# Kernel tuning notes

Hardware: AMD Instinct MI355X
Metric: run time of the kernel (lower is better)

Reference implementation:

```python
import jax, jax.numpy as jnp
import numpy as np

N_ATOMS = 4096
N_ANGLES = 200000


def setup_inputs() -> dict:
    key = jax.random.key(0)
    k1, k2, k3, k4, k5 = jax.random.split(key, 5)
    # pairwise unit direction vectors [N, N, 3]
    vec = jax.random.normal(k1, (N_ATOMS, N_ATOMS, 3), dtype=jnp.float32)
    vec = vec / jnp.linalg.norm(vec, axis=-1, keepdims=True)
    # pairwise distances [N, N], strictly positive
    dist = jax.random.uniform(k2, (N_ATOMS, N_ATOMS), dtype=jnp.float32) * 2.0 + 0.5
    # angle triplets [A, 3]
    coord_idx = jax.random.randint(k3, (N_ANGLES, 3), 0, N_ATOMS)
    # per-angle parameters: k0 (force const) and theta0 (equilibrium angle, rad)
    k0 = jax.random.uniform(k4, (N_ANGLES,), dtype=jnp.float32) * 100.0
    theta0 = jax.random.uniform(k5, (N_ANGLES,), dtype=jnp.float32) * np.float32(np.pi)
    params = jnp.stack([k0, theta0], axis=1)
    forces_out = jnp.zeros((N_ATOMS, 3), dtype=jnp.float32)
    return {
        "dist_mat": dist,
        "vector_mat": vec,
        "forces_out": forces_out,
        "params": params,
        "coord_idx": coord_idx,
        "calc_energy": 1,
        "calc_forces": 1,
    }


def reference(dist_mat, vector_mat, forces_out, params, coord_idx, calc_energy, calc_forces):
    k0 = params[:, 0]
    theta0 = params[:, 1]
    a1 = coord_idx[:, 0]
    a2 = coord_idx[:, 1]
    a3 = coord_idx[:, 2]

    vec21 = vector_mat[a2, a1]            # [A, 3]
    vec23 = vector_mat[a2, a3]            # [A, 3]
    dist21 = dist_mat[a2, a1]             # [A]
    dist23 = dist_mat[a2, a3]             # [A]

    cos_theta = jnp.clip(jnp.sum(vec21 * vec23, axis=1), -1.0, 1.0)
    theta = jnp.arccos(cos_theta)
    delta_theta = theta - theta0

    if calc_energy:
        energy = jnp.sum(k0 * delta_theta * delta_theta)
    else:
        energy = jnp.zeros([1], dtype=forces_out.dtype)

    forces = forces_out
    if calc_forces:
        sin_theta = jnp.sqrt(1.0 - cos_theta * cos_theta)
        # matches torch nan_to_num(nan=0.0): zero out coef where sin_theta == 0
        coef = jnp.where(sin_theta > 0.0,
                         -2.0 * k0 * delta_theta / jnp.maximum(sin_theta, 1e-12),
                         0.0)
        force0 = coef[:, None] * (cos_theta[:, None] * vec21 - vec23) / dist21[:, None]
        force2 = coef[:, None] * (cos_theta[:, None] * vec23 - vec21) / dist23[:, None]
        force1 = -(force0 + force2)
        forces = forces.at[a1].add(force0).at[a2].add(force1).at[a3].add(force2)

    return energy, forces
```

## Files before the change

kernel.cpp:

```cpp
#include <hip/hip_runtime.h>


#define NB 256
#define NT 1024

__global__ void init_out_kernel(float* __restrict__ out,
                                const float* __restrict__ forces0,
                                int nf) {
    int j = blockIdx.x * blockDim.x + threadIdx.x;
    if (j == 0) out[0] = 0.0f;
    if (j < nf) out[1 + j] = forces0[j];
}

template <bool USE_WS>
__global__ void __launch_bounds__(NT)
angle_fused_kernel(const float*  __restrict__ dist,
                   const float*  __restrict__ vec,
                   const float2* __restrict__ params,
                   const int*    __restrict__ cidx,
                   const int*    __restrict__ ce_p,
                   const int*    __restrict__ cf_p,
                   float* __restrict__ out,
                   float* __restrict__ ws_f,
                   float* __restrict__ ws_e,
                   int n_atoms, int n_angles) {
    extern __shared__ float s_f[];
    __shared__ float s_e;
    const int nf  = n_atoms * 3;
    const int tid = threadIdx.x;
    const int b   = blockIdx.x;

    for (int j = tid; j < nf; j += NT) s_f[j] = 0.0f;
    if (tid == 0) s_e = 0.0f;
    __syncthreads();

    const int ce = ce_p[0];
    const int cf = cf_p[0];

    const int i0 = (int)(((long)b * n_angles) / NB);
    const int i1 = (int)(((long)(b + 1) * n_angles) / NB);
    const int i  = i0 + tid;

    float e_acc = 0.0f;
    if (i < i1) {
        const int a1 = cidx[3 * i + 0];
        const int a2 = cidx[3 * i + 1];
        const int a3 = cidx[3 * i + 2];
        const float2 kt = params[i];

        const unsigned row = (unsigned)a2 * (unsigned)n_atoms;
        const unsigned b21 = row + (unsigned)a1;
        const unsigned b23 = row + (unsigned)a3;
        const float* __restrict__ p21 = vec + 3u * b21;
        const float* __restrict__ p23 = vec + 3u * b23;

        const float v21x = p21[0], v21y = p21[1], v21z = p21[2];
        const float v23x = p23[0], v23y = p23[1], v23z = p23[2];
        const float d21 = dist[b21];
        const float d23 = dist[b23];

        float c = v21x * v23x + v21y * v23y + v21z * v23z;
        c = fminf(1.0f, fmaxf(-1.0f, c));
        const float th  = acosf(c);
        const float dth = th - kt.y;

        if (ce) e_acc = kt.x * dth * dth;

        if (cf) {
            const float s2 = fmaxf(0.0f, 1.0f - c * c);
            const float s  = sqrtf(s2);
            const float coef = (s > 0.0f) ? (-2.0f * kt.x * dth / fmaxf(s, 1e-12f)) : 0.0f;
            const float i21 = coef / d21;
            const float i23 = coef / d23;

            const float f0x = i21 * (c * v21x - v23x);
            const float f0y = i21 * (c * v21y - v23y);
            const float f0z = i21 * (c * v21z - v23z);
            const float f2x = i23 * (c * v23x - v21x);
            const float f2y = i23 * (c * v23y - v21y);
            const float f2z = i23 * (c * v23z - v21z);

            atomicAdd(&s_f[a1 * 3 + 0], f0x);
            atomicAdd(&s_f[a1 * 3 + 1], f0y);
            atomicAdd(&s_f[a1 * 3 + 2], f0z);
            atomicAdd(&s_f[a2 * 3 + 0], -(f0x + f2x));
            atomicAdd(&s_f[a2 * 3 + 1], -(f0y + f2y));
            atomicAdd(&s_f[a2 * 3 + 2], -(f0z + f2z));
            atomicAdd(&s_f[a3 * 3 + 0], f2x);
            atomicAdd(&s_f[a3 * 3 + 1], f2y);
            atomicAdd(&s_f[a3 * 3 + 2], f2z);
        }
    }

    for (int off = 32; off > 0; off >>= 1)
        e_acc += __shfl_down(e_acc, off, 64);
    if ((tid & 63) == 0) atomicAdd(&s_e, e_acc);
    __syncthreads();

    if constexpr (USE_WS) {
        float* __restrict__ wp = ws_f + (size_t)b * nf;
        const float4* __restrict__ s4 = (const float4*)s_f;
        float4* __restrict__ w4 = (float4*)wp;
        const int nf4 = nf >> 2;
        for (int q = tid; q < nf4; q += NT) w4[q] = s4[q];
        for (int j = (nf4 << 2) + tid; j < nf; j += NT) wp[j] = s_f[j];
        if (tid == 0) ws_e[b] = s_e;
    } else {
        if (ce && tid == 0) atomicAdd(&out[0], s_e);
        if (cf) {
            const int base = (b * (nf / NB)) % nf;
            for (int jj = tid; jj < nf; jj += NT) {
                int j = jj + base;
                if (j >= nf) j -= nf;
                const float v = s_f[j];
                if (v != 0.0f) atomicAdd(&out[1 + j], v);
            }
        }
    }
}

__global__ void __launch_bounds__(256)
reduce_kernel(const float* __restrict__ ws_f,
              const float* __restrict__ ws_e,
              const float* __restrict__ forces0,
              const int*   __restrict__ ce_p,
              float* __restrict__ out,
              int nf) {
    const int t  = threadIdx.x;
    const int jj = t & 63;
    const int bg = t >> 6;
    const int j  = blockIdx.x * 64 + jj;

    __shared__ float s_p[4][64];
    __shared__ float s_e;

    float acc = 0.0f;
    if (j < nf) {
        const float* __restrict__ p = ws_f + (size_t)(bg * 64) * nf + j;
        #pragma unroll 16
        for (int b = 0; b < 64; ++b) acc += p[(size_t)b * nf];
    }
    s_p[bg][jj] = acc;

    float e = (blockIdx.x == 0) ? ws_e[t] : 0.0f;
    if (t == 0) s_e = 0.0f;
    __syncthreads();

    if (blockIdx.x == 0) {
        for (int off = 32; off > 0; off >>= 1) e += __shfl_down(e, off, 64);
        if ((t & 63) == 0) atomicAdd(&s_e, e);
    }
    if (bg == 0 && j < nf)
        out[1 + j] = forces0[j] + s_p[0][jj] + s_p[1][jj] + s_p[2][jj] + s_p[3][jj];
    __syncthreads();
    if (blockIdx.x == 0 && t == 0) out[0] = ce_p[0] ? s_e : 0.0f;
}

extern "C" void kernel_launch(void* const* d_in, const int* in_sizes, int n_in,
                              void* d_out, int out_size, void* d_ws, size_t ws_size,
                              hipStream_t stream) {
    const float*  dist    = (const float*)d_in[0];
    const float*  vec     = (const float*)d_in[1];
    const float*  forces0 = (const float*)d_in[2];
    const float2* params  = (const float2*)d_in[3];
    const int*    cidx    = (const int*)d_in[4];
    const int*    ce_p    = (const int*)d_in[5];
    const int*    cf_p    = (const int*)d_in[6];
    float* out = (float*)d_out;

    const int n_atoms  = in_sizes[2] / 3;
    const int n_angles = in_sizes[4] / 3;
    const int nf = n_atoms * 3;

    const size_t lds_bytes = (size_t)nf * sizeof(float);
    const size_t ws_need = ((size_t)NB * nf + NB) * sizeof(float);

    if (d_ws != nullptr && ws_size >= ws_need) {
        float* ws_f = (float*)d_ws;
        float* ws_e = ws_f + (size_t)NB * nf;
        angle_fused_kernel<true><<<NB, NT, lds_bytes, stream>>>(
            dist, vec, params, cidx, ce_p, cf_p, out, ws_f, ws_e,
            n_atoms, n_angles);
        const int rblocks = (nf + 63) / 64;
        reduce_kernel<<<rblocks, 256, 0, stream>>>(ws_f, ws_e, forces0,
                                                   ce_p, out, nf);
    } else {
        init_out_kernel<<<(nf + 1 + 255) / 256, 256, 0, stream>>>(out, forces0, nf);
        angle_fused_kernel<false><<<NB, NT, lds_bytes, stream>>>(
            dist, vec, params, cidx, ce_p, cf_p, out, nullptr, nullptr,
            n_atoms, n_angles);
    }
}
```

Measured before the change: 296.5 us.

## Halve block count, process two angles per thread, overlap gathers with LDS zeroing

Cuts the angle kernel to 128 blocks, each thread handling two angles. Index, parameter and matrix gathers are issued before the shared-memory zeroing barrier so their latency overlaps it, and zeroing uses float4 stores. The reduction kernel now sums half as many per-block partial force arrays, reducing workspace traffic at the cost of lower parallelism in the main kernel. The fallback path also gains a grid-stride loop, fixing the case where there are more angles than NB*NT.

```diff
diff --git a/kernel.cpp b/kernel.cpp
--- a/kernel.cpp
+++ b/kernel.cpp
@@ -1,8 +1,9 @@
 #include <hip/hip_runtime.h>
 
 
-#define NB 256
+#define NB 128
 #define NT 1024
+#define ANG 2
 
 __global__ void init_out_kernel(float* __restrict__ out,
                                 const float* __restrict__ forces0,
@@ -10,6 +11,46 @@
     int j = blockIdx.x * blockDim.x + threadIdx.x;
     if (j == 0) out[0] = 0.0f;
     if (j < nf) out[1 + j] = forces0[j];
+}
+
+__device__ __forceinline__ void angle_force(int ce, int cf,
+                                            float v21x, float v21y, float v21z,
+                                            float v23x, float v23y, float v23z,
+                                            float d21, float d23, float2 kt,
+                                            int a1, int a2, int a3,
+                                            float* __restrict__ s_f,
+                                            float& e_acc) {
+    float c = v21x * v23x + v21y * v23y + v21z * v23z;
+    c = fminf(1.0f, fmaxf(-1.0f, c));
+    const float th  = acosf(c);
+    const float dth = th - kt.y;
+
+    if (ce) e_acc += kt.x * dth * dth;
+
+    if (cf) {
+        const float s2 = fmaxf(0.0f, 1.0f - c * c);
+        const float s  = sqrtf(s2);
+        const float coef = (s > 0.0f) ? (-2.0f * kt.x * dth / fmaxf(s, 1e-12f)) : 0.0f;
+        const float i21 = coef / d21;
+        const float i23 = coef / d23;
+
+        const float f0x = i21 * (c * v21x - v23x);
+        const float f0y = i21 * (c * v21y - v23y);
+        const float f0z = i21 * (c * v21z - v23z);
+        const float f2x = i23 * (c * v23x - v21x);
+        const float f2y = i23 * (c * v23y - v21y);
+        const float f2z = i23 * (c * v23z - v21z);
+
+        atomicAdd(&s_f[a1 * 3 + 0], f0x);
+        atomicAdd(&s_f[a1 * 3 + 1], f0y);
+        atomicAdd(&s_f[a1 * 3 + 2], f0z);
+        atomicAdd(&s_f[a2 * 3 + 0], -(f0x + f2x));
+        atomicAdd(&s_f[a2 * 3 + 1], -(f0y + f2y));
+        atomicAdd(&s_f[a2 * 3 + 2], -(f0z + f2z));
+        atomicAdd(&s_f[a3 * 3 + 0], f2x);
+        atomicAdd(&s_f[a3 * 3 + 1], f2y);
+        atomicAdd(&s_f[a3 * 3 + 2], f2z);
+    }
 }
 
 template <bool USE_WS>
@@ -30,65 +71,86 @@
     const int tid = threadIdx.x;
     const int b   = blockIdx.x;
 
-    for (int j = tid; j < nf; j += NT) s_f[j] = 0.0f;
-    if (tid == 0) s_e = 0.0f;
-    __syncthreads();
+    const int i0 = (int)(((long)b * n_angles) / NB);
+    const int i1 = (int)(((long)(b + 1) * n_angles) / NB);
 
     const int ce = ce_p[0];
     const int cf = cf_p[0];
-
-    const int i0 = (int)(((long)b * n_angles) / NB);
-    const int i1 = (int)(((long)(b + 1) * n_angles) / NB);
-    const int i  = i0 + tid;
-
     float e_acc = 0.0f;
-    if (i < i1) {
-        const int a1 = cidx[3 * i + 0];
-        const int a2 = cidx[3 * i + 1];
-        const int a3 = cidx[3 * i + 2];
-        const float2 kt = params[i];
-
-        const unsigned row = (unsigned)a2 * (unsigned)n_atoms;
-        const unsigned b21 = row + (unsigned)a1;
-        const unsigned b23 = row + (unsigned)a3;
-        const float* __restrict__ p21 = vec + 3u * b21;
-        const float* __restrict__ p23 = vec + 3u * b23;
-
-        const float v21x = p21[0], v21y = p21[1], v21z = p21[2];
-        const float v23x = p23[0], v23y = p23[1], v23z = p23[2];
-        const float d21 = dist[b21];
-        const float d23 = dist[b23];
-
-        float c = v21x * v23x + v21y * v23y + v21z * v23z;
-        c = fminf(1.0f, fmaxf(-1.0f, c));
-        const float th  = acosf(c);
-        const float dth = th - kt.y;
-
-        if (ce) e_acc = kt.x * dth * dth;
-
-        if (cf) {
-            const float s2 = fmaxf(0.0f, 1.0f - c * c);
-            const float s  = sqrtf(s2);
-            const float coef = (s > 0.0f) ? (-2.0f * kt.x * dth / fmaxf(s, 1e-12f)) : 0.0f;
-            const float i21 = coef / d21;
-            const float i23 = coef / d23;
-
-            const float f0x = i21 * (c * v21x - v23x);
-            const float f0y = i21 * (c * v21y - v23y);
-            const float f0z = i21 * (c * v21z - v23z);
-            const float f2x = i23 * (c * v23x - v21x);
-            const float f2y = i23 * (c * v23y - v21y);
-            const float f2z = i23 * (c * v23z - v21z);
-
-            atomicAdd(&s_f[a1 * 3 + 0], f0x);
-            atomicAdd(&s_f[a1 * 3 + 1], f0y);
-            atomicAdd(&s_f[a1 * 3 + 2], f0z);
-            atomicAdd(&s_f[a2 * 3 + 0], -(f0x + f2x));
-            atomicAdd(&s_f[a2 * 3 + 1], -(f0y + f2y));
-            atomicAdd(&s_f[a2 * 3 + 2], -(f0z + f2z));
-            atomicAdd(&s_f[a3 * 3 + 0], f2x);
-            atomicAdd(&s_f[a3 * 3 + 1], f2y);
-            atomicAdd(&s_f[a3 * 3 + 2], f2z);
+
+    if constexpr (USE_WS) {
+        int    a1[ANG], a2[ANG], a3[ANG];
+        float2 kt[ANG];
+        bool   act[ANG];
+
+        #pragma unroll
+        for (int k = 0; k < ANG; ++k) {
+            const int i = i0 + tid + k * NT;
+            act[k] = (i < i1);
+            a1[k] = 0; a2[k] = 0; a3[k] = 0;
+            kt[k] = make_float2(0.0f, 0.0f);
+            if (act[k]) {
+                a1[k] = cidx[3 * i + 0];
+                a2[k] = cidx[3 * i + 1];
+                a3[k] = cidx[3 * i + 2];
+                kt[k] = params[i];
+            }
+        }
+
+        {
+            float4* __restrict__ s4 = (float4*)s_f;
+            const int nf4 = nf >> 2;
+            for (int q = tid; q < nf4; q += NT) s4[q] = make_float4(0.f, 0.f, 0.f, 0.f);
+            for (int j = (nf4 << 2) + tid; j < nf; j += NT) s_f[j] = 0.0f;
+            if (tid == 0) s_e = 0.0f;
+        }
+
+        float v21x[ANG], v21y[ANG], v21z[ANG], d21[ANG];
+        float v23x[ANG], v23y[ANG], v23z[ANG], d23[ANG];
+        #pragma unroll
+        for (int k = 0; k < ANG; ++k) {
+            v21x[k] = v21y[k] = v21z[k] = 0.f; d21[k] = 1.f;
+            v23x[k] = v23y[k] = v23z[k] = 0.f; d23[k] = 1.f;
+            if (act[k]) {
+                const unsigned row = (unsigned)a2[k] * (unsigned)n_atoms;
+                const unsigned b21 = row + (unsigned)a1[k];
+                const unsigned b23 = row + (unsigned)a3[k];
+                const float* __restrict__ p21 = vec + 3u * b21;
+                const float* __restrict__ p23 = vec + 3u * b23;
+                v21x[k] = p21[0]; v21y[k] = p21[1]; v21z[k] = p21[2];
+                v23x[k] = p23[0]; v23y[k] = p23[1]; v23z[k] = p23[2];
+                d21[k] = dist[b21];
+                d23[k] = dist[b23];
+            }
+        }
+
+        __syncthreads();
+
+        #pragma unroll
+        for (int k = 0; k < ANG; ++k) {
+            if (act[k])
+                angle_force(ce, cf, v21x[k], v21y[k], v21z[k],
+                            v23x[k], v23y[k], v23z[k], d21[k], d23[k],
+                            kt[k], a1[k], a2[k], a3[k], s_f, e_acc);
+        }
+    } else {
+        for (int j = tid; j < nf; j += NT) s_f[j] = 0.0f;
+        if (tid == 0) s_e = 0.0f;
+        __syncthreads();
+
+        for (int i = i0 + tid; i < i1; i += NT) {
+            const int a1 = cidx[3 * i + 0];
+            const int a2 = cidx[3 * i + 1];
+            const int a3 = cidx[3 * i + 2];
+            const float2 kt = params[i];
+            const unsigned row = (unsigned)a2 * (unsigned)n_atoms;
+            const unsigned b21 = row + (unsigned)a1;
+            const unsigned b23 = row + (unsigned)a3;
+            const float* __restrict__ p21 = vec + 3u * b21;
+            const float* __restrict__ p23 = vec + 3u * b23;
+            angle_force(ce, cf, p21[0], p21[1], p21[2],
+                        p23[0], p23[1], p23[2], dist[b21], dist[b23],
+                        kt, a1, a2, a3, s_f, e_acc);
         }
     }
 
@@ -136,13 +198,13 @@
 
     float acc = 0.0f;
     if (j < nf) {
-        const float* __restrict__ p = ws_f + (size_t)(bg * 64) * nf + j;
-        #pragma unroll 16
-        for (int b = 0; b < 64; ++b) acc += p[(size_t)b * nf];
+        const float* __restrict__ p = ws_f + (size_t)(bg * (NB / 4)) * nf + j;
+        #pragma unroll 8
+        for (int b = 0; b < NB / 4; ++b) acc += p[(size_t)b * nf];
     }
     s_p[bg][jj] = acc;
 
-    float e = (blockIdx.x == 0) ? ws_e[t] : 0.0f;
+    float e = (blockIdx.x == 0 && t < NB) ? ws_e[t] : 0.0f;
     if (t == 0) s_e = 0.0f;
     __syncthreads();
 
@@ -173,9 +235,13 @@
     const int nf = n_atoms * 3;
 
     const size_t lds_bytes = (size_t)nf * sizeof(float);
-    const size_t ws_need = ((size_t)NB * nf + NB) * sizeof(float);
-
-    if (d_ws != nullptr && ws_size >= ws_need) {
+    const size_t ws_need   = ((size_t)NB * nf + NB) * sizeof(float);
+
+    const bool main_ok = (d_ws != nullptr) && (ws_size >= ws_need) &&
+                         (n_angles <= NB * NT * ANG) &&
+                         (lds_bytes <= 160 * 1024 - 1024);
+
+    if (main_ok) {
         float* ws_f = (float*)d_ws;
         float* ws_e = ws_f + (size_t)NB * nf;
         angle_fused_kernel<true><<<NB, NT, lds_bytes, stream>>>(
```

New measurement: 313.2 us. 5.7% more time.
